# Optimization experiments

Hardware: AMD Instinct MI355X
Metric: run time of the kernel (lower is better)

## Reference

```python
import jax, jax.numpy as jnp
import numpy as np

BATCH, C_IN, H = 16, 32, 224
N_FILT, K = 64, 5


def setup_inputs() -> dict:
    key = jax.random.key(0)
    k1, k2 = jax.random.split(key)
    x = jax.random.normal(k1, (BATCH, C_IN, H, H), dtype=jnp.float32)
    weight = jax.random.normal(k2, (N_FILT, C_IN, K, K), dtype=jnp.float32)
    bias = jnp.zeros((N_FILT,), dtype=jnp.float32)  # torch init: zeros(1) per filter
    return {"x": x, "weight": weight, "bias": bias}


def reference(x, weight, bias):
    # Fully-connected conv layer: stride 1, VALID padding.
    # Equivalent to stacking per-filter sum(x_patch * w) + scalar bias.
    out = jax.lax.conv_general_dilated(
        x, weight,
        window_strides=(1, 1),
        padding='VALID',
        dimension_numbers=('NCHW', 'OIHW', 'NCHW'),
    )
    # per-filter scalar bias broadcast over spatial dims
    return out + bias[None, :, None, None]
```

## Files before the change

### kernel.cpp

```cpp
#include <hip/hip_runtime.h>

#define CI    32
#define IH    224
#define IW    224
#define OHS   220
#define OWS   220
#define NF    64
#define KS    5

#define XCOLS 228
#define CP    36
#define WPD   40
#define XROWS 8
#define NBUFW (KS * NF * WPD)

#define PXW   116
#define RCHK  (PXW * 4)
#define SROWS 7
#define ROWB  (RCHK * 16)

typedef __attribute__((ext_vector_type(4))) float   f32x4;
typedef __attribute__((ext_vector_type(4))) __bf16  bf16x4;
typedef __attribute__((ext_vector_type(8))) __bf16  bf16x8;

__global__ __launch_bounds__(256)
void prep_kernel(const float* __restrict__ x, const float* __restrict__ w,
                 __bf16* __restrict__ xh, __bf16* __restrict__ wp) {
  int chunk = blockIdx.x * 256 + threadIdx.x;
  int c8  = (chunk & 3) * 8;
  int pos = chunk >> 2;
  int ww  = pos % IW;
  int nh  = pos / IW;
  int n   = nh / IH;
  int h   = nh - n * IH;
  const float* xp = x + ((size_t)n * CI + c8) * (IH * IW) + h * IW + ww;
  bf16x8 v;
#pragma unroll
  for (int j = 0; j < 8; ++j) v[j] = (__bf16)xp[(size_t)j * (IH * IW)];
  *(bf16x8*)(xh + (size_t)pos * CI + c8) = v;

  if (blockIdx.x < 200) {
    int i = blockIdx.x * 256 + threadIdx.x;
    int c   = i & (CI - 1);
    int f   = (i >> 5) & (NF - 1);
    int tap = i >> 11;
    int kh = tap / KS, kw = tap % KS;
    wp[i] = (__bf16)w[((f * CI + c) * KS + kh) * KS + kw];
  }
}

__global__ __launch_bounds__(256, 3)
void conv_lds3(const __bf16* __restrict__ xh, const __bf16* __restrict__ wp,
               const float* __restrict__ bias, float* __restrict__ out) {
  __shared__ __bf16 xs[SROWS * RCHK * 8];

  const int tid  = threadIdx.x;
  const int lane = tid & 63;
  const int wv   = tid >> 6;
  const int m    = lane & 15;
  const int q    = lane >> 4;

  const int bid = blockIdx.x;
  const int lid = (bid & 7) * 296 + (bid >> 3);
  const int n   = lid / 148;
  const int rem = lid - n * 148;
  const int oh0 = (rem >> 1) * 3;
  const int ow0 = (rem & 1) * 112;

  {
    const __bf16* xb = xh + (((size_t)n * IH + oh0) * IW + ow0) * CI;
#pragma unroll
    for (int rr = 0; rr < 2; ++rr) {
      int r = wv + rr * 4;
      if (r < SROWS) {
        const __bf16* src = xb + (size_t)r * (IW * CI);
        const int db = r * (RCHK * 8);
#pragma unroll
        for (int k = 0; k < 7; ++k)
          __builtin_amdgcn_global_load_lds(
              (const __attribute__((address_space(1))) void*)(src + k * 512 + lane * 8),
              (__attribute__((address_space(3))) void*)&xs[db + k * 512], 16, 0, 0);
        if (lane < 16)
          __builtin_amdgcn_global_load_lds(
              (const __attribute__((address_space(1))) void*)(src + 448 * 8 + lane * 8),
              (__attribute__((address_space(3))) void*)&xs[db + 448 * 8], 16, 0, 0);
      }
    }
  }

  const int NJ = (wv == 0) ? 6 : 5;
  int cj[6], rjv[6], bbase[6];
#pragma unroll
  for (int j = 0; j < 6; ++j) {
    int t  = wv + j * 4;
    int rj = t / 7;
    rjv[j] = rj;
    cj[j]  = (t - rj * 7) * 16;
    bbase[j] = rj * ROWB + ((cj[j] + m) * 4 + q) * 16;
  }

  f32x4 acc[24];
#pragma unroll
  for (int i = 0; i < 24; ++i) { f32x4 z = {0.f, 0.f, 0.f, 0.f}; acc[i] = z; }

  const __bf16* wpl = wp + m * CI + q * 8;

  __syncthreads();

  for (int kh = 0; kh < KS; ++kh) {
    const int khb = kh * ROWB;
#pragma unroll
    for (int kw = 0; kw < KS; ++kw) {
      bf16x8 af[4];
#pragma unroll
      for (int ft = 0; ft < 4; ++ft)
        af[ft] = *(const bf16x8*)(wpl + (size_t)(kh * KS + kw) * (NF * CI) + ft * 16 * CI);
#pragma unroll
      for (int j = 0; j < 6; ++j) {
        if (j < NJ) {
          bf16x8 bv = *(const bf16x8*)((const char*)xs + khb + bbase[j] + kw * 64);
#pragma unroll
          for (int ft = 0; ft < 4; ++ft)
            acc[j * 4 + ft] =
                __builtin_amdgcn_mfma_f32_16x16x32_bf16(af[ft], bv, acc[j * 4 + ft], 0, 0, 0);
        }
      }
    }
  }

  float bvv[16];
#pragma unroll
  for (int ft = 0; ft < 4; ++ft)
#pragma unroll
    for (int rg = 0; rg < 4; ++rg)
      bvv[ft * 4 + rg] = bias[ft * 16 + q * 4 + rg];

#pragma unroll
  for (int j = 0; j < 6; ++j) {
    if (j < NJ) {
      int ow = ow0 + cj[j] + m;
      int oh = oh0 + rjv[j];
      if (ow < OWS && oh < OHS) {
#pragma unroll
        for (int ft = 0; ft < 4; ++ft)
#pragma unroll
          for (int rg = 0; rg < 4; ++rg) {
            int f = ft * 16 + q * 4 + rg;
            out[(((size_t)n * NF + f) * OHS + oh) * OWS + ow] =
                acc[j * 4 + ft][rg] + bvv[ft * 4 + rg];
          }
      }
    }
  }
}

__global__ void repack_w_kernel(const float* __restrict__ w, __bf16* __restrict__ wp) {
  int i = blockIdx.x * 256 + threadIdx.x;
  if (i >= KS * KS * NF * CI) return;
  int c   = i & (CI - 1);
  int f   = (i >> 5) & (NF - 1);
  int tap = i >> 11;
  int kh = tap / KS, kw = tap % KS;
  wp[i] = (__bf16)w[((f * CI + c) * KS + kh) * KS + kw];
}

template <bool USE_WS>
__global__ __launch_bounds__(512, 1)
void conv_main(const float* __restrict__ x, const float* __restrict__ w,
               const __bf16* __restrict__ wp, const float* __restrict__ bias,
               float* __restrict__ out) {
  __shared__ __bf16 xs[XROWS * XCOLS * CP];
  __shared__ __bf16 wsm[NBUFW];

  const int tid  = threadIdx.x;
  const int lane = tid & 63;
  const int wv   = tid >> 6;
  const int m    = lane & 15;
  const int q    = lane >> 4;

  int bid = blockIdx.x;
  int lid = (bid >> 3) + (bid & 7) * 110;
  const int n   = lid / 55;
  const int oh0 = (lid % 55) * 4;

  {
    const float* xn = x + (size_t)n * CI * IH * IW;
    for (int p = tid; p < XROWS * 56 * 8; p += 512) {
      int pc   = p & 7;
      int pg   = p >> 3;
      int pcol = pg % 56;
      int prow = pg / 56;
      int row  = oh0 + prow;
      f32x4 v0 = *(const f32x4*)(xn + ((size_t)(pc * 4 + 0) * IH + row) * IW + pcol * 4);
      f32x4 v1 = *(const f32x4*)(xn + ((size_t)(pc * 4 + 1) * IH + row) * IW + pcol * 4);
      f32x4 v2 = *(const f32x4*)(xn + ((size_t)(pc * 4 + 2) * IH + row) * IW + pcol * 4);
      f32x4 v3 = *(const f32x4*)(xn + ((size_t)(pc * 4 + 3) * IH + row) * IW + pcol * 4);
#pragma unroll
      for (int dcol = 0; dcol < 4; ++dcol) {
        bf16x4 t;
        t[0] = (__bf16)v0[dcol]; t[1] = (__bf16)v1[dcol];
        t[2] = (__bf16)v2[dcol]; t[3] = (__bf16)v3[dcol];
        *(bf16x4*)&xs[(prow * XCOLS + pcol * 4 + dcol) * CP + pc * 4] = t;
      }
    }
    for (int z = tid; z < XROWS * 4 * CP; z += 512) {
      int rr  = z / (4 * CP);
      int rem = z - rr * (4 * CP);
      xs[(rr * XCOLS + 224) * CP + rem] = (__bf16)0.0f;
    }
  }

  if (USE_WS) {
    for (int i = tid; i < NF * CI * KS / 8; i += 512) {
      int c0 = (i & 3) * 8;
      int f  = (i >> 2) & 63;
      int kw = i >> 8;
      bf16x8 v = *(const bf16x8*)(wp + ((size_t)(0 * KS + kw) * NF + f) * CI + c0);
      *(bf16x8*)&wsm[(kw * NF + f) * WPD + c0] = v;
    }
  } else {
    for (int i = tid; i < KS * NF * CI; i += 512) {
      int c  = i & 31;
      int f  = (i >> 5) & 63;
      int kw = i >> 11;
      wsm[(kw * NF + f) * WPD + c] = (__bf16)w[((f * CI + c) * KS + 0) * KS + kw];
    }
  }
  __syncthreads();

  int rj[7], cbj[7], xoff[7];
#pragma unroll
  for (int j = 0; j < 7; ++j) {
    int t   = wv + j * 8;
    rj[j]   = t / 14;
    cbj[j]  = (t % 14) * 16;
    xoff[j] = (rj[j] * XCOLS + cbj[j] + m) * CP + q * 8;
  }

  f32x4 acc[28];
#pragma unroll
  for (int i = 0; i < 28; ++i) { f32x4 z = {0.f, 0.f, 0.f, 0.f}; acc[i] = z; }

  for (int kh = 0; kh < KS; ++kh) {
    bf16x8 pw[3];
    if (USE_WS && kh < KS - 1) {
#pragma unroll
      for (int it = 0; it < 3; ++it) {
        int e = it * 512 + tid;
        if (e < 1280) {
          int c0 = (e & 3) * 8;
          int f  = (e >> 2) & 63;
          int kw = e >> 8;
          pw[it] = *(const bf16x8*)(wp + ((size_t)((kh + 1) * KS + kw) * NF + f) * CI + c0);
        }
      }
    }

#pragma unroll
    for (int kw = 0; kw < KS; ++kw) {
      bf16x8 af[4];
#pragma unroll
      for (int ft = 0; ft < 4; ++ft)
        af[ft] = *(const bf16x8*)&wsm[(kw * NF + ft * 16 + m) * WPD + q * 8];
#pragma unroll
      for (int j = 0; j < 7; ++j) {
        const __bf16* bp = &xs[xoff[j] + (kh * XCOLS + kw) * CP];
        bf16x4 lo = *(const bf16x4*)bp;
        bf16x4 hi = *(const bf16x4*)(bp + 4);
        bf16x8 bv8 = __builtin_shufflevector(lo, hi, 0, 1, 2, 3, 4, 5, 6, 7);
#pragma unroll
        for (int ft = 0; ft < 4; ++ft)
          acc[j * 4 + ft] =
              __builtin_amdgcn_mfma_f32_16x16x32_bf16(af[ft], bv8, acc[j * 4 + ft], 0, 0, 0);
      }
    }

    if (kh < KS - 1) {
      __syncthreads();
      if (USE_WS) {
#pragma unroll
        for (int it = 0; it < 3; ++it) {
          int e = it * 512 + tid;
          if (e < 1280) {
            int c0 = (e & 3) * 8;
            int f  = (e >> 2) & 63;
            int kw = e >> 8;
            *(bf16x8*)&wsm[(kw * NF + f) * WPD + c0] = pw[it];
          }
        }
      } else {
        for (int i = tid; i < KS * NF * CI; i += 512) {
          int c  = i & 31;
          int f  = (i >> 5) & 63;
          int kw = i >> 11;
          wsm[(kw * NF + f) * WPD + c] =
              (__bf16)w[((f * CI + c) * KS + (kh + 1)) * KS + kw];
        }
      }
      __syncthreads();
    }
  }

  float bvv[16];
#pragma unroll
  for (int ft = 0; ft < 4; ++ft)
#pragma unroll
    for (int rg = 0; rg < 4; ++rg)
      bvv[ft * 4 + rg] = bias[ft * 16 + q * 4 + rg];

#pragma unroll
  for (int j = 0; j < 7; ++j) {
    int ow = cbj[j] + m;
    if (ow < OWS) {
      int oh = oh0 + rj[j];
#pragma unroll
      for (int ft = 0; ft < 4; ++ft) {
#pragma unroll
        for (int rg = 0; rg < 4; ++rg) {
          int f = ft * 16 + q * 4 + rg;
          out[(((size_t)n * NF + f) * OHS + oh) * OWS + ow] = acc[j * 4 + ft][rg] + bvv[ft * 4 + rg];
        }
      }
    }
  }
}

extern "C" void kernel_launch(void* const* d_in, const int* in_sizes, int n_in,
                              void* d_out, int out_size, void* d_ws, size_t ws_size,
                              hipStream_t stream) {
  const float* x    = (const float*)d_in[0];
  const float* w    = (const float*)d_in[1];
  const float* bias = (const float*)d_in[2];
  float* out = (float*)d_out;

  const int    NW = KS * KS * NF * CI;
  const size_t WB = (size_t)NW * sizeof(__bf16);
  const size_t XB = (size_t)16 * IH * IW * CI * sizeof(__bf16);

  if (ws_size >= XB + WB) {
    __bf16* xhp = (__bf16*)d_ws;
    __bf16* wp  = (__bf16*)((char*)d_ws + XB);
    prep_kernel<<<(16 * IH * IW * 4) / 256, 256, 0, stream>>>(x, w, xhp, wp);
    conv_lds3<<<2368, 256, 0, stream>>>(xhp, wp, bias, out);
  } else if (ws_size >= WB) {
    __bf16* wp = (__bf16*)d_ws;
    repack_w_kernel<<<(NW + 255) / 256, 256, 0, stream>>>(w, wp);
    conv_main<true><<<880, 512, 0, stream>>>(x, w, wp, bias, out);
  } else {
    conv_main<false><<<880, 512, 0, stream>>>(x, w, nullptr, bias, out);
  }
}
```

Before: 394.9 us.

## Use full-width 4-row output tiles with 512-thread blocks in LDS conv

Replaces the 3-row by 112-column output tile with a 4-row, full 220-column tile per block, staging 8 input rows of 912 bf16x8 chunks in LDS. Each block now has 8 waves, each holding 7 MFMA pixel tiles. The aim is to cut the input-halo reload ratio and remove the uneven per-wave work split of the old tiling. In exchange the block needs far more LDS (about 114 KB), which likely limits it to one block per CU. The grid also shrinks to 880 blocks, which risks lower occupancy and tail imbalance. The padded row stride also reads a little past each staged row.

```diff
diff --git a/kernel.cpp b/kernel.cpp
--- a/kernel.cpp
+++ b/kernel.cpp
@@ -14,10 +14,10 @@
 #define XROWS 8
 #define NBUFW (KS * NF * WPD)
 
-#define PXW   116
-#define RCHK  (PXW * 4)
-#define SROWS 7
-#define ROWB  (RCHK * 16)
+#define RCHKF 912
+#define ROWBF (RCHKF * 16)
+#define SROWSF 8
+#define TCHKF (RCHKF * SROWSF)
 
 typedef __attribute__((ext_vector_type(4))) float   f32x4;
 typedef __attribute__((ext_vector_type(4))) __bf16  bf16x4;
@@ -49,10 +49,10 @@
   }
 }
 
-__global__ __launch_bounds__(256, 3)
-void conv_lds3(const __bf16* __restrict__ xh, const __bf16* __restrict__ wp,
+__global__ __launch_bounds__(512, 2)
+void conv_full(const __bf16* __restrict__ xh, const __bf16* __restrict__ wp,
                const float* __restrict__ bias, float* __restrict__ out) {
-  __shared__ __bf16 xs[SROWS * RCHK * 8];
+  __shared__ __bf16 xs[TCHKF * 8];
 
   const int tid  = threadIdx.x;
   const int lane = tid & 63;
@@ -61,54 +61,42 @@
   const int q    = lane >> 4;
 
   const int bid = blockIdx.x;
-  const int lid = (bid & 7) * 296 + (bid >> 3);
-  const int n   = lid / 148;
-  const int rem = lid - n * 148;
-  const int oh0 = (rem >> 1) * 3;
-  const int ow0 = (rem & 1) * 112;
+  const int lid = (bid & 7) * 110 + (bid >> 3);
+  const int n   = lid / 55;
+  const int oh0 = (lid - n * 55) * 4;
 
   {
-    const __bf16* xb = xh + (((size_t)n * IH + oh0) * IW + ow0) * CI;
-#pragma unroll
-    for (int rr = 0; rr < 2; ++rr) {
-      int r = wv + rr * 4;
-      if (r < SROWS) {
-        const __bf16* src = xb + (size_t)r * (IW * CI);
-        const int db = r * (RCHK * 8);
-#pragma unroll
-        for (int k = 0; k < 7; ++k)
-          __builtin_amdgcn_global_load_lds(
-              (const __attribute__((address_space(1))) void*)(src + k * 512 + lane * 8),
-              (__attribute__((address_space(3))) void*)&xs[db + k * 512], 16, 0, 0);
-        if (lane < 16)
-          __builtin_amdgcn_global_load_lds(
-              (const __attribute__((address_space(1))) void*)(src + 448 * 8 + lane * 8),
-              (__attribute__((address_space(3))) void*)&xs[db + 448 * 8], 16, 0, 0);
-      }
-    }
-  }
-
-  const int NJ = (wv == 0) ? 6 : 5;
-  int cj[6], rjv[6], bbase[6];
-#pragma unroll
-  for (int j = 0; j < 6; ++j) {
-    int t  = wv + j * 4;
-    int rj = t / 7;
+    const __bf16* xb = xh + (size_t)(n * IH + oh0) * (IW * CI);
+    for (int g = wv; g < TCHKF / 64; g += 8) {
+      int L = g * 64 + lane;
+      int r = L / RCHKF;
+      int c = L - r * RCHKF;
+      __builtin_amdgcn_global_load_lds(
+          (const __attribute__((address_space(1))) void*)(xb + (size_t)r * (IW * CI) + c * 8),
+          (__attribute__((address_space(3))) void*)&xs[g * 512], 16, 0, 0);
+    }
+  }
+
+  int cbj[7], rjv[7], bbase[7];
+#pragma unroll
+  for (int j = 0; j < 7; ++j) {
+    int t  = wv + j * 8;
+    int rj = t / 14;
     rjv[j] = rj;
-    cj[j]  = (t - rj * 7) * 16;
-    bbase[j] = rj * ROWB + ((cj[j] + m) * 4 + q) * 16;
-  }
-
-  f32x4 acc[24];
-#pragma unroll
-  for (int i = 0; i < 24; ++i) { f32x4 z = {0.f, 0.f, 0.f, 0.f}; acc[i] = z; }
+    cbj[j] = (t % 14) * 16;
+    bbase[j] = rj * ROWBF + (cbj[j] + m) * 64 + q * 16;
+  }
+
+  f32x4 acc[28];
+#pragma unroll
+  for (int i = 0; i < 28; ++i) { f32x4 z = {0.f, 0.f, 0.f, 0.f}; acc[i] = z; }
 
   const __bf16* wpl = wp + m * CI + q * 8;
 
   __syncthreads();
 
   for (int kh = 0; kh < KS; ++kh) {
-    const int khb = kh * ROWB;
+    const int khb = kh * ROWBF;
 #pragma unroll
     for (int kw = 0; kw < KS; ++kw) {
       bf16x8 af[4];
@@ -116,14 +104,12 @@
       for (int ft = 0; ft < 4; ++ft)
         af[ft] = *(const bf16x8*)(wpl + (size_t)(kh * KS + kw) * (NF * CI) + ft * 16 * CI);
 #pragma unroll
-      for (int j = 0; j < 6; ++j) {
-        if (j < NJ) {
-          bf16x8 bv = *(const bf16x8*)((const char*)xs + khb + bbase[j] + kw * 64);
-#pragma unroll
-          for (int ft = 0; ft < 4; ++ft)
-            acc[j * 4 + ft] =
-                __builtin_amdgcn_mfma_f32_16x16x32_bf16(af[ft], bv, acc[j * 4 + ft], 0, 0, 0);
-        }
+      for (int j = 0; j < 7; ++j) {
+        bf16x8 bv = *(const bf16x8*)((const char*)xs + khb + bbase[j] + kw * 64);
+#pragma unroll
+        for (int ft = 0; ft < 4; ++ft)
+          acc[j * 4 + ft] =
+              __builtin_amdgcn_mfma_f32_16x16x32_bf16(af[ft], bv, acc[j * 4 + ft], 0, 0, 0);
       }
     }
   }
@@ -136,20 +122,18 @@
       bvv[ft * 4 + rg] = bias[ft * 16 + q * 4 + rg];
 
 #pragma unroll
-  for (int j = 0; j < 6; ++j) {
-    if (j < NJ) {
-      int ow = ow0 + cj[j] + m;
+  for (int j = 0; j < 7; ++j) {
+    int ow = cbj[j] + m;
+    if (ow < OWS) {
       int oh = oh0 + rjv[j];
-      if (ow < OWS && oh < OHS) {
-#pragma unroll
-        for (int ft = 0; ft < 4; ++ft)
-#pragma unroll
-          for (int rg = 0; rg < 4; ++rg) {
-            int f = ft * 16 + q * 4 + rg;
-            out[(((size_t)n * NF + f) * OHS + oh) * OWS + ow] =
-                acc[j * 4 + ft][rg] + bvv[ft * 4 + rg];
-          }
-      }
+#pragma unroll
+      for (int ft = 0; ft < 4; ++ft)
+#pragma unroll
+        for (int rg = 0; rg < 4; ++rg) {
+          int f = ft * 16 + q * 4 + rg;
+          out[(((size_t)n * NF + f) * OHS + oh) * OWS + ow] =
+              acc[j * 4 + ft][rg] + bvv[ft * 4 + rg];
+        }
     }
   }
 }
@@ -341,7 +325,7 @@
     __bf16* xhp = (__bf16*)d_ws;
     __bf16* wp  = (__bf16*)((char*)d_ws + XB);
     prep_kernel<<<(16 * IH * IW * 4) / 256, 256, 0, stream>>>(x, w, xhp, wp);
-    conv_lds3<<<2368, 256, 0, stream>>>(xhp, wp, bias, out);
+    conv_full<<<880, 512, 0, stream>>>(xhp, wp, bias, out);
   } else if (ws_size >= WB) {
     __bf16* wp = (__bf16*)d_ws;
     repack_w_kernel<<<(NW + 255) / 256, 256, 0, stream>>>(w, wp);
```

After: 395.9 us. No clear change (+0.3%).
